# Kernel tuning notes

Hardware: AMD Instinct MI355X
Metric: run time of the kernel (lower is better)

Reference implementation:

```python
import jax, jax.numpy as jnp
import numpy as np

DIM = 128
WINDOW_TOKENS = 64  # window_size**2 = 8*8


def _conv3x3(x, w):
    # x: [B,C,H,W], w: [O,I,3,3], padding=1 (SAME)
    return jax.lax.conv_general_dilated(
        x, w, window_strides=(1, 1), padding='SAME',
        dimension_numbers=('NCHW', 'OIHW', 'NCHW'))


def _pixel_shuffle2(x):
    # torch.nn.PixelShuffle(2): [B, C*4, H, W] -> [B, C, 2H, 2W]
    B, C4, H, W = x.shape
    C = C4 // 4
    x = x.reshape(B, C, 2, 2, H, W)
    x = x.transpose(0, 1, 4, 2, 5, 3)  # [B, C, H, 2, W, 2]
    return x.reshape(B, C, H * 2, W * 2)


def setup_inputs() -> dict:
    key = jax.random.key(0)
    ks = jax.random.split(key, 12)
    B, C = 4, DIM
    f0 = jax.random.normal(ks[0], (B, C, 64, 64), jnp.float32)
    f1 = jax.random.normal(ks[1], (B, C, 128, 128), jnp.float32)
    f2 = jax.random.normal(ks[2], (B, C, 256, 256), jnp.float32)
    s = 0.02
    # Linear weights stored as [in, out] so forward is x @ W
    Wq = jax.random.normal(ks[3], (C, C), jnp.float32) * s
    Wk = jax.random.normal(ks[4], (C, C), jnp.float32) * s
    Wv = jax.random.normal(ks[5], (C, C), jnp.float32) * s
    Wql = jax.random.normal(ks[6], (C, C), jnp.float32) * s
    Wkl = jax.random.normal(ks[7], (C, C), jnp.float32) * s
    Wvl = jax.random.normal(ks[8], (C, C), jnp.float32) * s
    gate_w = jax.random.normal(ks[9], (2 * C, C), jnp.float32) * s
    conv0 = jax.random.normal(ks[10], (4 * C, C, 3, 3), jnp.float32) * s
    conv1 = jax.random.normal(ks[11], (4 * C, C, 3, 3), jnp.float32) * s
    return dict(f0=f0, f1=f1, f2=f2, Wq=Wq, Wk=Wk, Wv=Wv,
                Wql=Wql, Wkl=Wkl, Wvl=Wvl, gate_w=gate_w,
                conv0=conv0, conv1=conv1)


def reference(f0, f1, f2, Wq, Wk, Wv, Wql, Wkl, Wvl, gate_w, conv0, conv1):
    feats = (f0, f1, f2)
    B, C = f0.shape[0], f0.shape[1]
    scale = C ** (-0.5)
    # flatten+concat: [B, N, C]
    toks = [f.reshape(B, C, -1).transpose(0, 2, 1) for f in feats]
    x = jnp.concatenate(toks, axis=1)
    N = x.shape[1]
    wt = WINDOW_TOKENS
    nw = N // wt  # N is divisible by wt for these shapes (no padding)
    windows = x.reshape(B, nw, wt, C)

    # ---- global path (mode='center'): attention over window means ----
    centers = windows.mean(axis=2)  # [B, nw, C]
    Q = centers @ Wq
    K = centers @ Wk
    V = centers @ Wv
    attn = jax.nn.softmax(jnp.einsum('bnc,bmc->bnm', Q, K) * scale, axis=-1)
    y_centers = jnp.einsum('bnm,bmc->bnc', attn, V) * centers
    y_global = jnp.broadcast_to(y_centers[:, :, None, :], (B, nw, wt, C)).reshape(B, N, C)

    # ---- local path: attention within each window (batched over windows) ----
    Ql = windows @ Wql
    Kl = windows @ Wkl
    Vl = windows @ Wvl
    attn_l = jax.nn.softmax(jnp.einsum('bwqc,bwkc->bwqk', Ql, Kl) * scale, axis=-1)
    y_local = (jnp.einsum('bwqk,bwkc->bwqc', attn_l, Vl) * windows).reshape(B, N, C)

    # ---- gated fusion ----
    alpha = jax.nn.sigmoid(jnp.concatenate([y_global, y_local], axis=-1) @ gate_w)
    y = alpha * y_global + (1.0 - alpha) * y_local

    # ---- reshape back to feature maps ----
    maps = []
    start = 0
    for f in feats:
        H, W = f.shape[2], f.shape[3]
        cnt = H * W
        maps.append(y[:, start:start + cnt, :].transpose(0, 2, 1).reshape(B, C, H, W))
        start += cnt
    # ---- inverse wavelet reconstruction (conv3x3 -> pixel shuffle -> add) ----
    outputs = [maps[0]]
    z = maps[0]
    z = _pixel_shuffle2(_conv3x3(z, conv0)) + maps[1]
    outputs.append(z)
    z = _pixel_shuffle2(_conv3x3(z, conv1)) + maps[2]
    outputs.append(z)
    return tuple(outputs)
```

## Files before the change

### kernel.cpp

```cpp
#include <hip/hip_runtime.h>
#include <math.h>

#define WT 64
#define NWIN 1344
#define NP 1408
constexpr float SCALE = 0.088388347648318447f;

#define OUT0 0
#define OUT1 2097152
#define OUT2 10485760

typedef __attribute__((ext_vector_type(8))) short bfrag;
typedef __attribute__((ext_vector_type(8))) _Float16 hfrag;
typedef __attribute__((ext_vector_type(4))) float f32x4;

#define MFMA16 __builtin_amdgcn_mfma_f32_16x16x32_bf16
#define MFMA16H __builtin_amdgcn_mfma_f32_16x16x32_f16

__device__ __forceinline__ unsigned short f2b(float f) {
    union { float f; unsigned u; } v; v.f = f;
    unsigned r = v.u + 0x7fffu + ((v.u >> 16) & 1u);
    return (unsigned short)(r >> 16);
}
__device__ __forceinline__ float b2f(unsigned short u) {
    union { unsigned u; float f; } v; v.u = ((unsigned)u) << 16; return v.f;
}
__device__ __forceinline__ int pack2(float a, float b) {
    return (int)f2b(a) | ((int)f2b(b) << 16);
}

__device__ __forceinline__ bfrag ld256(const char* region, int row, int k) {
    int off = (2 * k) ^ ((row & 7) << 4);
    return *(const bfrag*)(region + row * 256 + off);
}
__device__ __forceinline__ bfrag ld128(const char* region, int row, int k) {
    int off = (2 * k) ^ ((row & 7) << 4);
    return *(const bfrag*)(region + row * 128 + off);
}

__global__ void k_prep(const float* __restrict__ Wql, const float* __restrict__ Wkl,
                       const float* __restrict__ Wvl, const float* __restrict__ gw,
                       const float* __restrict__ Wq, const float* __restrict__ Wk,
                       const float* __restrict__ Wv,
                       unsigned short* __restrict__ MtB,
                       unsigned short* __restrict__ WvltB,
                       unsigned short* __restrict__ G1tB,
                       unsigned short* __restrict__ G0tB,
                       unsigned short* __restrict__ MgtB,
                       unsigned short* __restrict__ WvtB) {
    int n = blockIdx.x, k = threadIdx.x;
    if (blockIdx.y == 0) {
        float a = 0.f;
        for (int c = 0; c < 128; ++c) a += Wkl[n * 128 + c] * Wql[k * 128 + c];
        MtB[n * 128 + k] = f2b(a);
    } else if (blockIdx.y == 1) {
        WvltB[n * 128 + k] = f2b(Wvl[k * 128 + n]);
    } else if (blockIdx.y == 2) {
        G1tB[n * 128 + k] = f2b(gw[(128 + k) * 128 + n]);
    } else if (blockIdx.y == 3) {
        G0tB[n * 128 + k] = f2b(gw[k * 128 + n]);
    } else if (blockIdx.y == 4) {
        float a = 0.f;
        for (int c = 0; c < 128; ++c) a += Wk[n * 128 + c] * Wq[k * 128 + c];
        MgtB[n * 128 + k] = f2b(a);
    } else {
        WvtB[n * 128 + k] = f2b(Wv[k * 128 + n]);
    }
}

__global__ __launch_bounds__(256) void k_prep_conv(
    const float* __restrict__ w0, const float* __restrict__ w1,
    _Float16* __restrict__ W0, _Float16* __restrict__ W1) {
    int idx = blockIdx.x * 256 + threadIdx.x;
    const float* w = blockIdx.y ? w1 : w0;
    _Float16* o = blockIdx.y ? W1 : W0;
    int slice = idx >> 14, rem = idx & 16383;
    int oc = rem >> 5, k = rem & 31;
    int ics = slice / 9, tap = slice - ics * 9;
    o[idx] = (_Float16)w[((size_t)oc * 128 + ics * 32 + k) * 9 + tap];
}

__device__ __forceinline__ void window_src(int n0, const float* f0, const float* f1,
                                           const float* f2, const float*& f, int& p0,
                                           int& HW, int& obase) {
    if (n0 < 4096)        { f = f0; p0 = n0;          HW = 4096;  obase = OUT0; }
    else if (n0 < 20480)  { f = f1; p0 = n0 - 4096;   HW = 16384; obase = OUT1; }
    else                  { f = f2; p0 = n0 - 20480;  HW = 65536; obase = OUT2; }
}

__global__ __launch_bounds__(256) void k_centers(
    const float* __restrict__ f0, const float* __restrict__ f1,
    const float* __restrict__ f2, float* __restrict__ ctr,
    unsigned short* __restrict__ ctrb) {
    int w = blockIdx.x, b = blockIdx.y;
    const float* f; int p0, HW, ob;
    window_src(w * WT, f0, f1, f2, f, p0, HW, ob);
    int lane = threadIdx.x & 63, cg = threadIdx.x >> 6;
    for (int c = cg; c < 128; c += 4) {
        float v = f[(b * 128 + c) * HW + p0 + lane];
        #pragma unroll
        for (int off = 32; off; off >>= 1) v += __shfl_xor(v, off);
        if (lane == 0) {
            float mv = v * (1.0f / 64.0f);
            ctr[(b * NWIN + w) * 128 + c] = mv;
            ctrb[(b * NWIN + w) * 128 + c] = f2b(mv);
        }
    }
}

__global__ __launch_bounds__(256) void k_tgvg2(
    const unsigned short* __restrict__ ctrb, const unsigned short* __restrict__ MgtB,
    const unsigned short* __restrict__ WvtB, unsigned short* __restrict__ Tgb,
    unsigned short* __restrict__ Vgt) {
    int blk = blockIdx.x, b = blockIdx.y;
    int mb = blk * 32;
    int tid = threadIdx.x, wid = tid >> 6, lane = tid & 63;
    int lr = lane & 15, lg = lane >> 4;
    int nb = wid * 32;
    f32x4 tg[2][2] = {};
    f32x4 vg[2][2] = {};
    const unsigned short* Cb = ctrb + ((size_t)b * NWIN + mb) * 128;
    #pragma unroll
    for (int ks = 0; ks < 4; ++ks) {
        int k = ks * 32 + lg * 8;
        bfrag b0 = *(const bfrag*)(Cb + lr * 128 + k);
        bfrag b1 = *(const bfrag*)(Cb + (16 + lr) * 128 + k);
        bfrag m0 = *(const bfrag*)(MgtB + (nb + lr) * 128 + k);
        bfrag m1 = *(const bfrag*)(MgtB + (nb + 16 + lr) * 128 + k);
        bfrag v0 = *(const bfrag*)(WvtB + (nb + lr) * 128 + k);
        bfrag v1 = *(const bfrag*)(WvtB + (nb + 16 + lr) * 128 + k);
        tg[0][0] = MFMA16(m0, b0, tg[0][0], 0, 0, 0);
        tg[0][1] = MFMA16(m0, b1, tg[0][1], 0, 0, 0);
        tg[1][0] = MFMA16(m1, b0, tg[1][0], 0, 0, 0);
        tg[1][1] = MFMA16(m1, b1, tg[1][1], 0, 0, 0);
        vg[0][0] = MFMA16(v0, b0, vg[0][0], 0, 0, 0);
        vg[0][1] = MFMA16(v0, b1, vg[0][1], 0, 0, 0);
        vg[1][0] = MFMA16(v1, b0, vg[1][0], 0, 0, 0);
        vg[1][1] = MFMA16(v1, b1, vg[1][1], 0, 0, 0);
    }
    #pragma unroll
    for (int ni = 0; ni < 2; ++ni)
        #pragma unroll
        for (int mj = 0; mj < 2; ++mj) {
            int n0 = nb + ni * 16 + 4 * lg;
            int m = mb + mj * 16 + lr;
            int2 tv;
            tv.x = pack2(tg[ni][mj][0], tg[ni][mj][1]);
            tv.y = pack2(tg[ni][mj][2], tg[ni][mj][3]);
            *(int2*)(Tgb + ((size_t)b * NWIN + m) * 128 + n0) = tv;
            #pragma unroll
            for (int r = 0; r < 4; ++r)
                Vgt[((size_t)b * 128 + n0 + r) * NP + m] = f2b(vg[ni][mj][r]);
        }
}

__global__ __launch_bounds__(256, 1) void k_qk(
    const unsigned short* __restrict__ Tgb, const unsigned short* __restrict__ ctrb,
    unsigned short* __restrict__ P) {
    extern __shared__ unsigned short Srow[];
    __shared__ float mxs[32], invs[32];
    int blk = blockIdx.x, b = blockIdx.y;
    int mb = blk * 32;
    int tid = threadIdx.x, wid = tid >> 6, lane = tid & 63;
    int lr = lane & 15, lg = lane >> 4;
    int wm = (wid & 1) * 16, wn = (wid >> 1) * 32;

    const unsigned short* Arow = Tgb + ((size_t)b * NWIN + mb + wm + lr) * 128;
    for (int tile = 0; tile < 21; ++tile) {
        int nb = tile * 64 + wn;
        f32x4 acc[2] = {};
        #pragma unroll
        for (int ks = 0; ks < 4; ++ks) {
            int k = ks * 32 + lg * 8;
            bfrag a = *(const bfrag*)(Arow + k);
            #pragma unroll
            for (int nt = 0; nt < 2; ++nt) {
                bfrag bb = *(const bfrag*)(ctrb + ((size_t)b * NWIN + nb + nt * 16 + lr) * 128 + k);
                acc[nt] = MFMA16(a, bb, acc[nt], 0, 0, 0);
            }
        }
        #pragma unroll
        for (int nt = 0; nt < 2; ++nt) {
            int col = nb + nt * 16 + lr;
            #pragma unroll
            for (int r = 0; r < 4; ++r) {
                int mrow = wm + 4 * lg + r;
                Srow[mrow * 1344 + col] = f2b(acc[nt][r]);
            }
        }
    }
    __syncthreads();
    {
        int row = tid >> 3, sub = tid & 7;
        const unsigned short* sr = Srow + row * 1344;
        float mx = -1e30f;
        for (int c = sub; c < 1344; c += 8) mx = fmaxf(mx, b2f(sr[c]));
        mx = fmaxf(mx, __shfl_xor(mx, 1));
        mx = fmaxf(mx, __shfl_xor(mx, 2));
        mx = fmaxf(mx, __shfl_xor(mx, 4));
        float sum = 0.f;
        for (int c = sub; c < 1344; c += 8) sum += __expf((b2f(sr[c]) - mx) * SCALE);
        sum += __shfl_xor(sum, 1);
        sum += __shfl_xor(sum, 2);
        sum += __shfl_xor(sum, 4);
        if (sub == 0) { mxs[row] = mx; invs[row] = 1.0f / sum; }
    }
    __syncthreads();
    unsigned short* Pb = P + ((size_t)b * NWIN + mb) * NP;
    for (int idx = tid; idx < 32 * (NP / 8); idx += 256) {
        int row = idx / (NP / 8), c8 = idx % (NP / 8);
        float mx = mxs[row], inv = invs[row];
        unsigned short o[8];
        #pragma unroll
        for (int e = 0; e < 8; ++e) {
            int c = c8 * 8 + e;
            float p = (c < 1344) ? __expf((b2f(Srow[row * 1344 + c]) - mx) * SCALE) * inv : 0.f;
            o[e] = f2b(p);
        }
        *(int4*)(Pb + row * NP + c8 * 8) = *(int4*)o;
    }
}

__global__ __launch_bounds__(256) void k_pvg0(
    const unsigned short* __restrict__ P, const unsigned short* __restrict__ Vgt,
    const float* __restrict__ ctr, const unsigned short* __restrict__ G0tB,
    float* __restrict__ ycen, float* __restrict__ g0g) {
    __shared__ __align__(16) char Ys[32 * 256];
    int blk = blockIdx.x, b = blockIdx.y;
    int mb = blk * 32;
    int tid = threadIdx.x, wid = tid >> 6, lane = tid & 63;
    int lr = lane & 15, lg = lane >> 4;
    int cb = wid * 32;
    f32x4 acc[2][2] = {};
    const unsigned short* Pb = P + ((size_t)b * NWIN + mb) * NP;
    const unsigned short* Vb = Vgt + (size_t)b * 128 * NP;
    for (int it = 0; it < 44; ++it) {
        int k = it * 32 + lg * 8;
        bfrag a0 = *(const bfrag*)(Vb + (size_t)(cb + lr) * NP + k);
        bfrag a1 = *(const bfrag*)(Vb + (size_t)(cb + 16 + lr) * NP + k);
        bfrag b0 = *(const bfrag*)(Pb + (size_t)lr * NP + k);
        bfrag b1 = *(const bfrag*)(Pb + (size_t)(16 + lr) * NP + k);
        acc[0][0] = MFMA16(a0, b0, acc[0][0], 0, 0, 0);
        acc[0][1] = MFMA16(a0, b1, acc[0][1], 0, 0, 0);
        acc[1][0] = MFMA16(a1, b0, acc[1][0], 0, 0, 0);
        acc[1][1] = MFMA16(a1, b1, acc[1][1], 0, 0, 0);
    }
    #pragma unroll
    for (int ci = 0; ci < 2; ++ci)
        #pragma unroll
        for (int mj = 0; mj < 2; ++mj) {
            int c0 = cb + ci * 16 + 4 * lg;
            int mr = mj * 16 + lr;
            int m = mb + mr;
            size_t base = ((size_t)b * NWIN + m) * 128 + c0;
            float4 cv = *(const float4*)(ctr + base);
            float4 y;
            y.x = acc[ci][mj][0] * cv.x;
            y.y = acc[ci][mj][1] * cv.y;
            y.z = acc[ci][mj][2] * cv.z;
            y.w = acc[ci][mj][3] * cv.w;
            *(float4*)(ycen + base) = y;
            int2 pv; pv.x = pack2(y.x, y.y); pv.y = pack2(y.z, y.w);
            *(int2*)(Ys + mr * 256 + ((2 * c0) ^ ((mr & 7) << 4))) = pv;
        }
    __syncthreads();
    {
        int nb = wid * 32;
        f32x4 g[2][2] = {};
        #pragma unroll
        for (int ks = 0; ks < 4; ++ks) {
            int k = ks * 32 + lg * 8;
            bfrag a0 = *(const bfrag*)(G0tB + (nb + lr) * 128 + k);
            bfrag a1 = *(const bfrag*)(G0tB + (nb + 16 + lr) * 128 + k);
            bfrag b0 = ld256(Ys, lr, k);
            bfrag b1 = ld256(Ys, 16 + lr, k);
            g[0][0] = MFMA16(a0, b0, g[0][0], 0, 0, 0);
            g[0][1] = MFMA16(a0, b1, g[0][1], 0, 0, 0);
            g[1][0] = MFMA16(a1, b0, g[1][0], 0, 0, 0);
            g[1][1] = MFMA16(a1, b1, g[1][1], 0, 0, 0);
        }
        #pragma unroll
        for (int ni = 0; ni < 2; ++ni)
            #pragma unroll
            for (int mj = 0; mj < 2; ++mj) {
                int m = mb + mj * 16 + lr;
                int n0 = nb + ni * 16 + 4 * lg;
                #pragma unroll
                for (int r = 0; r < 4; ++r)
                    g0g[((size_t)b * NWIN + m) * 128 + n0 + r] = g[ni][mj][r];
            }
    }
}

#define XB_OFF 0
#define WT_OFF 16384
#define XM_OFF 49152
#define VT_OFF 65536
#define SMEM_SZ 81920

__global__ __launch_bounds__(256, 2) void k_local_mfma(
    const float* __restrict__ f0, const float* __restrict__ f1,
    const float* __restrict__ f2,
    const unsigned short* __restrict__ MtB,
    const unsigned short* __restrict__ WvltB,
    const unsigned short* __restrict__ G1tB,
    const float* __restrict__ g0g, const float* __restrict__ ycen,
    float* __restrict__ out) {
    extern __shared__ char smem[];
    char* Xb = smem + XB_OFF;
    char* Wt = smem + WT_OFF;
    char* XMb = smem + XM_OFF;
    char* Vt = smem + VT_OFF;

    int w = blockIdx.x, b = blockIdx.y;
    const float* f; int p0, HW, obase;
    window_src(w * WT, f0, f1, f2, f, p0, HW, obase);

    int tid = threadIdx.x;
    int wid = tid >> 6, lane = tid & 63;
    int lr = lane & 15, lg = lane >> 4;

    {
        int t0 = tid & 63, cq = tid >> 6;
        const float* src = f + (size_t)(b * 128 + cq * 32) * HW + p0 + t0;
        float xv[32];
        #pragma unroll
        for (int i = 0; i < 32; ++i) xv[i] = src[(size_t)i * HW];
        int4 wreg[8];
        const int4* wsrc = (const int4*)MtB;
        #pragma unroll
        for (int j = 0; j < 8; ++j) wreg[j] = wsrc[j * 256 + tid];
        #pragma unroll
        for (int j = 0; j < 4; ++j) {
            int c0 = cq * 32 + j * 8;
            int4 v;
            v.x = pack2(xv[j * 8 + 0], xv[j * 8 + 1]);
            v.y = pack2(xv[j * 8 + 2], xv[j * 8 + 3]);
            v.z = pack2(xv[j * 8 + 4], xv[j * 8 + 5]);
            v.w = pack2(xv[j * 8 + 6], xv[j * 8 + 7]);
            *(int4*)(Xb + t0 * 256 + ((2 * c0) ^ ((t0 & 7) << 4))) = v;
        }
        #pragma unroll
        for (int j = 0; j < 8; ++j) {
            int ci = j * 256 + tid, n = ci >> 4, pos = ci & 15;
            *(int4*)(Wt + n * 256 + ((pos * 16) ^ ((n & 7) << 4))) = wreg[j];
        }
    }
    __syncthreads();

    int t = 16 * wid + lr;

    {
        f32x4 acc[8] = {};
        #pragma unroll
        for (int ks = 0; ks < 4; ++ks) {
            int k = ks * 32 + lg * 8;
            bfrag xb = ld256(Xb, t, k);
            #pragma unroll
            for (int ct = 0; ct < 8; ++ct) {
                bfrag am = ld256(Wt, 16 * ct + lr, k);
                acc[ct] = MFMA16(am, xb, acc[ct], 0, 0, 0);
            }
        }
        #pragma unroll
        for (int ct = 0; ct < 8; ++ct) {
            int c0 = 16 * ct + 4 * lg;
            int2 v; v.x = pack2(acc[ct][0], acc[ct][1]); v.y = pack2(acc[ct][2], acc[ct][3]);
            *(int2*)(XMb + t * 256 + ((2 * c0) ^ ((t & 7) << 4))) = v;
        }
    }
    __syncthreads();

    {
        int4 wreg[8];
        const int4* wsrc = (const int4*)WvltB;
        #pragma unroll
        for (int j = 0; j < 8; ++j) wreg[j] = wsrc[j * 256 + tid];

        f32x4 s[4] = {};
        #pragma unroll
        for (int ks = 0; ks < 4; ++ks) {
            int k = ks * 32 + lg * 8;
            bfrag bxm = ld256(XMb, t, k);
            #pragma unroll
            for (int ut = 0; ut < 4; ++ut) {
                bfrag ax = ld256(Xb, 16 * ut + lr, k);
                s[ut] = MFMA16(ax, bxm, s[ut], 0, 0, 0);
            }
        }
        float m = -1e30f;
        #pragma unroll
        for (int ut = 0; ut < 4; ++ut)
            #pragma unroll
            for (int r = 0; r < 4; ++r) m = fmaxf(m, s[ut][r]);
        m = fmaxf(m, __shfl_xor(m, 16));
        m = fmaxf(m, __shfl_xor(m, 32));
        float sum = 0.f;
        float e[4][4];
        #pragma unroll
        for (int ut = 0; ut < 4; ++ut)
            #pragma unroll
            for (int r = 0; r < 4; ++r) {
                e[ut][r] = __expf((s[ut][r] - m) * SCALE);
                sum += e[ut][r];
            }
        sum += __shfl_xor(sum, 16);
        sum += __shfl_xor(sum, 32);
        float pinv = 1.0f / sum;
        #pragma unroll
        for (int ut = 0; ut < 4; ++ut) {
            int u0 = 16 * ut + 4 * lg;
            int2 v;
            v.x = pack2(e[ut][0] * pinv, e[ut][1] * pinv);
            v.y = pack2(e[ut][2] * pinv, e[ut][3] * pinv);
            *(int2*)(XMb + t * 256 + ((2 * u0) ^ ((t & 7) << 4))) = v;
        }
        #pragma unroll
        for (int j = 0; j < 8; ++j) {
            int ci = j * 256 + tid, n = ci >> 4, pos = ci & 15;
            *(int4*)(Wt + n * 256 + ((pos * 16) ^ ((n & 7) << 4))) = wreg[j];
        }
    }
    __syncthreads();

    int4 wregG[8];
    {
        const int4* wsrc = (const int4*)G1tB;
        #pragma unroll
        for (int j = 0; j < 8; ++j) wregG[j] = wsrc[j * 256 + tid];

        f32x4 vacc[8] = {};
        #pragma unroll
        for (int ks = 0; ks < 4; ++ks) {
            int k = ks * 32 + lg * 8;
            bfrag ax = ld256(Xb, t, k);
            #pragma unroll
            for (int ct = 0; ct < 8; ++ct) {
                bfrag bw = ld256(Wt, 16 * ct + lr, k);
                vacc[ct] = MFMA16(ax, bw, vacc[ct], 0, 0, 0);
            }
        }
        #pragma unroll
        for (int ct = 0; ct < 8; ++ct) {
            int c = 16 * ct + lr;
            int u0 = 16 * wid + 4 * lg;
            int2 v; v.x = pack2(vacc[ct][0], vacc[ct][1]); v.y = pack2(vacc[ct][2], vacc[ct][3]);
            *(int2*)(Vt + c * 128 + ((2 * u0) ^ ((c & 7) << 4))) = v;
        }
    }
    __syncthreads();

    float yl[8][4];
    float4 yg4[8], g04[8];
    {
        #pragma unroll
        for (int j = 0; j < 8; ++j) {
            int ci = j * 256 + tid, n = ci >> 4, pos = ci & 15;
            *(int4*)(Wt + n * 256 + ((pos * 16) ^ ((n & 7) << 4))) = wregG[j];
        }
        size_t rbase = ((size_t)b * NWIN + w) * 128 + 4 * lg;
        #pragma unroll
        for (int nt = 0; nt < 8; ++nt) {
            yg4[nt] = *(const float4*)(ycen + rbase + 16 * nt);
            g04[nt] = *(const float4*)(g0g + rbase + 16 * nt);
        }
        f32x4 y[8] = {};
        #pragma unroll
        for (int us = 0; us < 2; ++us) {
            int u = us * 32 + lg * 8;
            bfrag bp = ld256(XMb, t, u);
            #pragma unroll
            for (int ct = 0; ct < 8; ++ct) {
                bfrag av = ld128(Vt, 16 * ct + lr, u);
                y[ct] = MFMA16(av, bp, y[ct], 0, 0, 0);
            }
        }
        #pragma unroll
        for (int ct = 0; ct < 8; ++ct) {
            int c0 = 16 * ct + 4 * lg;
            int2 xw = *(const int2*)(Xb + t * 256 + ((2 * c0) ^ ((t & 7) << 4)));
            float x0 = b2f((unsigned short)(xw.x & 0xffff));
            float x1 = b2f((unsigned short)((unsigned)xw.x >> 16));
            float x2 = b2f((unsigned short)(xw.y & 0xffff));
            float x3 = b2f((unsigned short)((unsigned)xw.y >> 16));
            yl[ct][0] = y[ct][0] * x0;
            yl[ct][1] = y[ct][1] * x1;
            yl[ct][2] = y[ct][2] * x2;
            yl[ct][3] = y[ct][3] * x3;
            int2 v; v.x = pack2(yl[ct][0], yl[ct][1]); v.y = pack2(yl[ct][2], yl[ct][3]);
            *(int2*)(Xb + t * 256 + ((2 * c0) ^ ((t & 7) << 4))) = v;
        }
    }
    __syncthreads();

    {
        f32x4 g[8] = {};
        #pragma unroll
        for (int ks = 0; ks < 4; ++ks) {
            int k = ks * 32 + lg * 8;
            bfrag byl = ld256(Xb, t, k);
            #pragma unroll
            for (int nt = 0; nt < 8; ++nt) {
                bfrag ag = ld256(Wt, 16 * nt + lr, k);
                g[nt] = MFMA16(ag, byl, g[nt], 0, 0, 0);
            }
        }
        #pragma unroll
        for (int nt = 0; nt < 8; ++nt) {
            float gv[4] = {g04[nt].x, g04[nt].y, g04[nt].z, g04[nt].w};
            float yv4[4] = {yg4[nt].x, yg4[nt].y, yg4[nt].z, yg4[nt].w};
            #pragma unroll
            for (int r = 0; r < 4; ++r) {
                int c = 16 * nt + 4 * lg + r;
                float a = 1.0f / (1.0f + __expf(-(g[nt][r] + gv[r])));
                float yv = a * yv4[r] + (1.0f - a) * yl[nt][r];
                out[obase + (size_t)(b * 128 + c) * HW + p0 + t] = yv;
            }
        }
    }
}

template <int H, int W>
__global__ __launch_bounds__(256, 2) void k_conv_mfma(
    const float* __restrict__ in, const _Float16* __restrict__ Wcv,
    float* __restrict__ out) {
    constexpr int TXN = W / 32;
    int tile = blockIdx.x;
    int ty = tile / TXN, tx = tile % TXN;
    int y0 = ty * 4, x0 = tx * 32;
    int ob = blockIdx.y * 256;
    int b = blockIdx.z;

    __shared__ __align__(16) char sXs[16384];

    int tid = threadIdx.x;
    int wid = tid >> 6, lane = tid & 63;
    int lr = lane & 15, lg = lane >> 4;

    f32x4 acc[8][4] = {};

    int sy = tid / 34, sx = tid - sy * 34;
    int gy = y0 + sy - 1, gx = x0 + sx - 1;
    bool act = tid < 204;
    bool ok = act && gy >= 0 && gy < H && gx >= 0 && gx < W;
    const float* gp = in + (size_t)b * 128 * H * W + (size_t)gy * W + gx;
    int xswz = (tid >> 3) & 1;

    const _Float16* wbase = Wcv + (size_t)(ob + lr) * 32 + lg * 8;

    hfrag afC[4], afN[4];
    #pragma unroll
    for (int n = 0; n < 4; ++n)
        afC[n] = *(const hfrag*)(wbase + (size_t)(wid * 4 + n) * 512);

    if (act) {
        float xv[32];
        if (ok) {
            #pragma unroll
            for (int ic = 0; ic < 32; ++ic) xv[ic] = gp[(size_t)ic * H * W];
        } else {
            #pragma unroll
            for (int ic = 0; ic < 32; ++ic) xv[ic] = 0.f;
        }
        #pragma unroll
        for (int s = 0; s < 4; ++s) {
            _Float16 hh[8];
            #pragma unroll
            for (int e = 0; e < 8; ++e) hh[e] = (_Float16)xv[s * 8 + e];
            *(int4*)(sXs + tid * 80 + ((s ^ xswz) << 4)) = *(int4*)hh;
        }
    }
    __syncthreads();

    for (int ics = 0; ics < 4; ++ics) {
        if (ics) {
            __syncthreads();
            if (act) {
                float xv[32];
                if (ok) {
                    #pragma unroll
                    for (int ic = 0; ic < 32; ++ic)
                        xv[ic] = gp[(size_t)(ics * 32 + ic) * H * W];
                } else {
                    #pragma unroll
                    for (int ic = 0; ic < 32; ++ic) xv[ic] = 0.f;
                }
                #pragma unroll
                for (int s = 0; s < 4; ++s) {
                    _Float16 hh[8];
                    #pragma unroll
                    for (int e = 0; e < 8; ++e) hh[e] = (_Float16)xv[s * 8 + e];
                    *(int4*)(sXs + tid * 80 + ((s ^ xswz) << 4)) = *(int4*)hh;
                }
            }
            __syncthreads();
        }
        #pragma unroll
        for (int tap = 0; tap < 9; ++tap) {
            int kg = ics * 9 + tap;
            if (tap < 8 || ics < 3) {
                const _Float16* ws = wbase + (size_t)(kg + 1) * 16384;
                #pragma unroll
                for (int n = 0; n < 4; ++n)
                    afN[n] = *(const hfrag*)(ws + (size_t)(wid * 4 + n) * 512);
            }
            int dy = tap / 3, dx = tap - dy * 3;
            hfrag bf[8];
            #pragma unroll
            for (int m = 0; m < 8; ++m) {
                int row = ((m >> 1) + dy) * 34 + (m & 1) * 16 + lr + dx;
                bf[m] = *(const hfrag*)(sXs + row * 80 + ((lg ^ ((row >> 3) & 1)) << 4));
            }
            #pragma unroll
            for (int m = 0; m < 8; ++m)
                #pragma unroll
                for (int n = 0; n < 4; ++n)
                    acc[m][n] = MFMA16H(afC[n], bf[m], acc[m][n], 0, 0, 0);
            #pragma unroll
            for (int n = 0; n < 4; ++n) afC[n] = afN[n];
        }
    }

    float* outb = out + (size_t)b * 128 * 4 * H * W;
    #pragma unroll
    for (int n = 0; n < 4; ++n) {
        int oc0 = ob + (wid * 4 + n) * 16 + lg * 4;
        int c = oc0 >> 2;
        #pragma unroll
        for (int mr = 0; mr < 4; ++mr) {
            int py = y0 + mr;
            #pragma unroll
            for (int i2 = 0; i2 < 2; ++i2) {
                size_t rowb = ((size_t)c * (2 * H) + 2 * py + i2) * (2 * W);
                float2* p0 = (float2*)(outb + rowb + 2 * (x0 + lr));
                float2 v0 = *p0;
                v0.x += acc[2 * mr][n][i2 * 2 + 0];
                v0.y += acc[2 * mr][n][i2 * 2 + 1];
                *p0 = v0;
                float2* p1 = (float2*)(outb + rowb + 2 * (x0 + 16 + lr));
                float2 v1 = *p1;
                v1.x += acc[2 * mr + 1][n][i2 * 2 + 0];
                v1.y += acc[2 * mr + 1][n][i2 * 2 + 1];
                *p1 = v1;
            }
        }
    }
}

extern "C" void kernel_launch(void* const* d_in, const int* in_sizes, int n_in,
                              void* d_out, int out_size, void* d_ws, size_t ws_size,
                              hipStream_t stream) {
    const float* f0 = (const float*)d_in[0];
    const float* f1 = (const float*)d_in[1];
    const float* f2 = (const float*)d_in[2];
    const float* Wq = (const float*)d_in[3];
    const float* Wk = (const float*)d_in[4];
    const float* Wv = (const float*)d_in[5];
    const float* Wql = (const float*)d_in[6];
    const float* Wkl = (const float*)d_in[7];
    const float* Wvl = (const float*)d_in[8];
    const float* gate_w = (const float*)d_in[9];
    const float* conv0 = (const float*)d_in[10];
    const float* conv1 = (const float*)d_in[11];
    float* out = (float*)d_out;
    float* ws = (float*)d_ws;

    float* ctr = ws;
    float* ycen = ctr + 688128;
    float* g0g = ycen + 688128;
    unsigned short* MtB = (unsigned short*)(g0g + 688128);
    unsigned short* WvltB = MtB + 16384;
    unsigned short* G1tB = WvltB + 16384;
    unsigned short* G0tB = G1tB + 16384;
    unsigned short* MgtB = G0tB + 16384;
    unsigned short* WvtB = MgtB + 16384;
    _Float16* Wcv0 = (_Float16*)(WvtB + 16384);
    _Float16* Wcv1 = Wcv0 + 589824;
    unsigned short* ctrb = (unsigned short*)(Wcv1 + 589824);
    unsigned short* Tgb = ctrb + 688128;
    unsigned short* Vgt = Tgb + 688128;
    unsigned short* Pg = Vgt + 4 * 128 * NP;

    hipFuncSetAttribute((const void*)k_local_mfma,
                        hipFuncAttributeMaxDynamicSharedMemorySize, SMEM_SZ);
    hipFuncSetAttribute((const void*)k_qk,
                        hipFuncAttributeMaxDynamicSharedMemorySize, 32 * 1344 * 2);

    k_prep<<<dim3(128, 6), 128, 0, stream>>>(Wql, Wkl, Wvl, gate_w, Wq, Wk, Wv,
                                             MtB, WvltB, G1tB, G0tB, MgtB, WvtB);
    k_prep_conv<<<dim3(2304, 2), 256, 0, stream>>>(conv0, conv1, Wcv0, Wcv1);
    k_centers<<<dim3(NWIN, 4), 256, 0, stream>>>(f0, f1, f2, ctr, ctrb);
    k_tgvg2<<<dim3(NWIN / 32, 4), 256, 0, stream>>>(ctrb, MgtB, WvtB, Tgb, Vgt);
    k_qk<<<dim3(NWIN / 32, 4), 256, 32 * 1344 * 2, stream>>>(Tgb, ctrb, Pg);
    k_pvg0<<<dim3(NWIN / 32, 4), 256, 0, stream>>>(Pg, Vgt, ctr, G0tB, ycen, g0g);
    k_local_mfma<<<dim3(NWIN, 4), 256, SMEM_SZ, stream>>>(
        f0, f1, f2, MtB, WvltB, G1tB, g0g, ycen, out);
    k_conv_mfma<64, 64><<<dim3(32, 2, 4), 256, 0, stream>>>(out + OUT0, Wcv0, out + OUT1);
    k_conv_mfma<128, 128><<<dim3(128, 2, 4), 256, 0, stream>>>(out + OUT1, Wcv1, out + OUT2);
}
```

Measured before the change: 568.7 us.

## Fuse global-path QK, softmax and PV into one kernel keeping P in LDS

Merges the global attention score, softmax and PV+gate kernels into a single kernel that keeps the probability matrix in shared memory. The Q·M projection is now computed in-block into LDS instead of being written to a global Tgb buffer. This removes the global round trips for P and Tgb and one kernel launch. In exchange it uses more LDS per block, pads the row stride to reduce bank conflicts, and serializes the stages within a block. This global path is a small part of total time, which is dominated by the local and conv kernels.

```diff
diff --git a/kernel.cpp b/kernel.cpp
--- a/kernel.cpp
+++ b/kernel.cpp
@@ -4,6 +4,7 @@
 #define WT 64
 #define NWIN 1344
 #define NP 1408
+#define SROW_STRIDE 1352
 constexpr float SCALE = 0.088388347648318447f;
 
 #define OUT0 0
@@ -108,16 +109,14 @@
     }
 }
 
-__global__ __launch_bounds__(256) void k_tgvg2(
-    const unsigned short* __restrict__ ctrb, const unsigned short* __restrict__ MgtB,
-    const unsigned short* __restrict__ WvtB, unsigned short* __restrict__ Tgb,
+__global__ __launch_bounds__(256) void k_vg(
+    const unsigned short* __restrict__ ctrb, const unsigned short* __restrict__ WvtB,
     unsigned short* __restrict__ Vgt) {
     int blk = blockIdx.x, b = blockIdx.y;
     int mb = blk * 32;
     int tid = threadIdx.x, wid = tid >> 6, lane = tid & 63;
     int lr = lane & 15, lg = lane >> 4;
     int nb = wid * 32;
-    f32x4 tg[2][2] = {};
     f32x4 vg[2][2] = {};
     const unsigned short* Cb = ctrb + ((size_t)b * NWIN + mb) * 128;
     #pragma unroll
@@ -125,14 +124,8 @@
         int k = ks * 32 + lg * 8;
         bfrag b0 = *(const bfrag*)(Cb + lr * 128 + k);
         bfrag b1 = *(const bfrag*)(Cb + (16 + lr) * 128 + k);
-        bfrag m0 = *(const bfrag*)(MgtB + (nb + lr) * 128 + k);
-        bfrag m1 = *(const bfrag*)(MgtB + (nb + 16 + lr) * 128 + k);
         bfrag v0 = *(const bfrag*)(WvtB + (nb + lr) * 128 + k);
         bfrag v1 = *(const bfrag*)(WvtB + (nb + 16 + lr) * 128 + k);
-        tg[0][0] = MFMA16(m0, b0, tg[0][0], 0, 0, 0);
-        tg[0][1] = MFMA16(m0, b1, tg[0][1], 0, 0, 0);
-        tg[1][0] = MFMA16(m1, b0, tg[1][0], 0, 0, 0);
-        tg[1][1] = MFMA16(m1, b1, tg[1][1], 0, 0, 0);
         vg[0][0] = MFMA16(v0, b0, vg[0][0], 0, 0, 0);
         vg[0][1] = MFMA16(v0, b1, vg[0][1], 0, 0, 0);
         vg[1][0] = MFMA16(v1, b0, vg[1][0], 0, 0, 0);
@@ -144,55 +137,86 @@
         for (int mj = 0; mj < 2; ++mj) {
             int n0 = nb + ni * 16 + 4 * lg;
             int m = mb + mj * 16 + lr;
-            int2 tv;
-            tv.x = pack2(tg[ni][mj][0], tg[ni][mj][1]);
-            tv.y = pack2(tg[ni][mj][2], tg[ni][mj][3]);
-            *(int2*)(Tgb + ((size_t)b * NWIN + m) * 128 + n0) = tv;
             #pragma unroll
             for (int r = 0; r < 4; ++r)
                 Vgt[((size_t)b * 128 + n0 + r) * NP + m] = f2b(vg[ni][mj][r]);
         }
 }
 
-__global__ __launch_bounds__(256, 1) void k_qk(
-    const unsigned short* __restrict__ Tgb, const unsigned short* __restrict__ ctrb,
-    unsigned short* __restrict__ P) {
-    extern __shared__ unsigned short Srow[];
+#define QKPV_LDS (32 * SROW_STRIDE * 2 + 8192)
+
+__global__ __launch_bounds__(256, 1) void k_qkpv(
+    const unsigned short* __restrict__ ctrb, const unsigned short* __restrict__ MgtB,
+    const unsigned short* __restrict__ Vgt, const unsigned short* __restrict__ G0tB,
+    const float* __restrict__ ctr, float* __restrict__ ycen,
+    float* __restrict__ g0g) {
+    extern __shared__ char smem2[];
+    unsigned short* Srow = (unsigned short*)smem2;
+    char* Ys = smem2 + 32 * SROW_STRIDE * 2;
     __shared__ float mxs[32], invs[32];
     int blk = blockIdx.x, b = blockIdx.y;
     int mb = blk * 32;
     int tid = threadIdx.x, wid = tid >> 6, lane = tid & 63;
     int lr = lane & 15, lg = lane >> 4;
-    int wm = (wid & 1) * 16, wn = (wid >> 1) * 32;
-
-    const unsigned short* Arow = Tgb + ((size_t)b * NWIN + mb + wm + lr) * 128;
-    for (int tile = 0; tile < 21; ++tile) {
-        int nb = tile * 64 + wn;
-        f32x4 acc[2] = {};
+
+    {
+        int nb = wid * 32;
+        f32x4 tg[2][2] = {};
+        const unsigned short* Cb = ctrb + ((size_t)b * NWIN + mb) * 128;
         #pragma unroll
         for (int ks = 0; ks < 4; ++ks) {
             int k = ks * 32 + lg * 8;
-            bfrag a = *(const bfrag*)(Arow + k);
+            bfrag b0 = *(const bfrag*)(Cb + lr * 128 + k);
+            bfrag b1 = *(const bfrag*)(Cb + (16 + lr) * 128 + k);
+            bfrag m0 = *(const bfrag*)(MgtB + (nb + lr) * 128 + k);
+            bfrag m1 = *(const bfrag*)(MgtB + (nb + 16 + lr) * 128 + k);
+            tg[0][0] = MFMA16(m0, b0, tg[0][0], 0, 0, 0);
+            tg[0][1] = MFMA16(m0, b1, tg[0][1], 0, 0, 0);
+            tg[1][0] = MFMA16(m1, b0, tg[1][0], 0, 0, 0);
+            tg[1][1] = MFMA16(m1, b1, tg[1][1], 0, 0, 0);
+        }
+        #pragma unroll
+        for (int ni = 0; ni < 2; ++ni)
+            #pragma unroll
+            for (int mj = 0; mj < 2; ++mj) {
+                int n0 = nb + ni * 16 + 4 * lg;
+                int m = mj * 16 + lr;
+                int2 v; v.x = pack2(tg[ni][mj][0], tg[ni][mj][1]);
+                v.y = pack2(tg[ni][mj][2], tg[ni][mj][3]);
+                *(int2*)(Ys + m * 256 + ((2 * n0) ^ ((m & 7) << 4))) = v;
+            }
+    }
+    __syncthreads();
+
+    {
+        int wm = (wid & 1) * 16, wn = (wid >> 1) * 32;
+        for (int tile = 0; tile < 21; ++tile) {
+            int nb = tile * 64 + wn;
+            f32x4 acc[2] = {};
+            #pragma unroll
+            for (int ks = 0; ks < 4; ++ks) {
+                int k = ks * 32 + lg * 8;
+                bfrag a = ld256(Ys, wm + lr, k);
+                #pragma unroll
+                for (int nt = 0; nt < 2; ++nt) {
+                    bfrag bb = *(const bfrag*)(ctrb + ((size_t)b * NWIN + nb + nt * 16 + lr) * 128 + k);
+                    acc[nt] = MFMA16(a, bb, acc[nt], 0, 0, 0);
+                }
+            }
             #pragma unroll
             for (int nt = 0; nt < 2; ++nt) {
-                bfrag bb = *(const bfrag*)(ctrb + ((size_t)b * NWIN + nb + nt * 16 + lr) * 128 + k);
-                acc[nt] = MFMA16(a, bb, acc[nt], 0, 0, 0);
-            }
-        }
-        #pragma unroll
-        for (int nt = 0; nt < 2; ++nt) {
-            int col = nb + nt * 16 + lr;
-            #pragma unroll
-            for (int r = 0; r < 4; ++r) {
-                int mrow = wm + 4 * lg + r;
-                Srow[mrow * 1344 + col] = f2b(acc[nt][r]);
-            }
-        }
-    }
-    __syncthreads();
+                int col = nb + nt * 16 + lr;
+                #pragma unroll
+                for (int r = 0; r < 4; ++r)
+                    Srow[(wm + 4 * lg + r) * SROW_STRIDE + col] = f2b(acc[nt][r]);
+            }
+        }
+    }
+    __syncthreads();
+
     {
         int row = tid >> 3, sub = tid & 7;
-        const unsigned short* sr = Srow + row * 1344;
+        const unsigned short* sr = Srow + row * SROW_STRIDE;
         float mx = -1e30f;
         for (int c = sub; c < 1344; c += 8) mx = fmaxf(mx, b2f(sr[c]));
         mx = fmaxf(mx, __shfl_xor(mx, 1));
@@ -206,64 +230,57 @@
         if (sub == 0) { mxs[row] = mx; invs[row] = 1.0f / sum; }
     }
     __syncthreads();
-    unsigned short* Pb = P + ((size_t)b * NWIN + mb) * NP;
-    for (int idx = tid; idx < 32 * (NP / 8); idx += 256) {
-        int row = idx / (NP / 8), c8 = idx % (NP / 8);
+    for (int idx = tid; idx < 32 * (SROW_STRIDE / 8); idx += 256) {
+        int row = idx / (SROW_STRIDE / 8), c8 = idx % (SROW_STRIDE / 8);
         float mx = mxs[row], inv = invs[row];
+        unsigned short* sp = Srow + row * SROW_STRIDE + c8 * 8;
         unsigned short o[8];
         #pragma unroll
         for (int e = 0; e < 8; ++e) {
             int c = c8 * 8 + e;
-            float p = (c < 1344) ? __expf((b2f(Srow[row * 1344 + c]) - mx) * SCALE) * inv : 0.f;
+            float p = (c < 1344) ? __expf((b2f(sp[e]) - mx) * SCALE) * inv : 0.f;
             o[e] = f2b(p);
         }
-        *(int4*)(Pb + row * NP + c8 * 8) = *(int4*)o;
-    }
-}
-
-__global__ __launch_bounds__(256) void k_pvg0(
-    const unsigned short* __restrict__ P, const unsigned short* __restrict__ Vgt,
-    const float* __restrict__ ctr, const unsigned short* __restrict__ G0tB,
-    float* __restrict__ ycen, float* __restrict__ g0g) {
-    __shared__ __align__(16) char Ys[32 * 256];
-    int blk = blockIdx.x, b = blockIdx.y;
-    int mb = blk * 32;
-    int tid = threadIdx.x, wid = tid >> 6, lane = tid & 63;
-    int lr = lane & 15, lg = lane >> 4;
-    int cb = wid * 32;
-    f32x4 acc[2][2] = {};
-    const unsigned short* Pb = P + ((size_t)b * NWIN + mb) * NP;
-    const unsigned short* Vb = Vgt + (size_t)b * 128 * NP;
-    for (int it = 0; it < 44; ++it) {
-        int k = it * 32 + lg * 8;
-        bfrag a0 = *(const bfrag*)(Vb + (size_t)(cb + lr) * NP + k);
-        bfrag a1 = *(const bfrag*)(Vb + (size_t)(cb + 16 + lr) * NP + k);
-        bfrag b0 = *(const bfrag*)(Pb + (size_t)lr * NP + k);
-        bfrag b1 = *(const bfrag*)(Pb + (size_t)(16 + lr) * NP + k);
-        acc[0][0] = MFMA16(a0, b0, acc[0][0], 0, 0, 0);
-        acc[0][1] = MFMA16(a0, b1, acc[0][1], 0, 0, 0);
-        acc[1][0] = MFMA16(a1, b0, acc[1][0], 0, 0, 0);
-        acc[1][1] = MFMA16(a1, b1, acc[1][1], 0, 0, 0);
-    }
-    #pragma unroll
-    for (int ci = 0; ci < 2; ++ci)
-        #pragma unroll
-        for (int mj = 0; mj < 2; ++mj) {
-            int c0 = cb + ci * 16 + 4 * lg;
-            int mr = mj * 16 + lr;
-            int m = mb + mr;
-            size_t base = ((size_t)b * NWIN + m) * 128 + c0;
-            float4 cv = *(const float4*)(ctr + base);
-            float4 y;
-            y.x = acc[ci][mj][0] * cv.x;
-            y.y = acc[ci][mj][1] * cv.y;
-            y.z = acc[ci][mj][2] * cv.z;
-            y.w = acc[ci][mj][3] * cv.w;
-            *(float4*)(ycen + base) = y;
-            int2 pv; pv.x = pack2(y.x, y.y); pv.y = pack2(y.z, y.w);
-            *(int2*)(Ys + mr * 256 + ((2 * c0) ^ ((mr & 7) << 4))) = pv;
-        }
-    __syncthreads();
+        *(int4*)sp = *(int4*)o;
+    }
+    __syncthreads();
+
+    {
+        int cb = wid * 32;
+        f32x4 acc[2][2] = {};
+        const unsigned short* Vb = Vgt + (size_t)b * 128 * NP;
+        for (int it = 0; it < 42; ++it) {
+            int k = it * 32 + lg * 8;
+            bfrag a0 = *(const bfrag*)(Vb + (size_t)(cb + lr) * NP + k);
+            bfrag a1 = *(const bfrag*)(Vb + (size_t)(cb + 16 + lr) * NP + k);
+            bfrag b0 = *(const bfrag*)(Srow + lr * SROW_STRIDE + k);
+            bfrag b1 = *(const bfrag*)(Srow + (16 + lr) * SROW_STRIDE + k);
+            acc[0][0] = MFMA16(a0, b0, acc[0][0], 0, 0, 0);
+            acc[0][1] = MFMA16(a0, b1, acc[0][1], 0, 0, 0);
+            acc[1][0] = MFMA16(a1, b0, acc[1][0], 0, 0, 0);
+            acc[1][1] = MFMA16(a1, b1, acc[1][1], 0, 0, 0);
+        }
+        #pragma unroll
+        for (int ci = 0; ci < 2; ++ci)
+            #pragma unroll
+            for (int mj = 0; mj < 2; ++mj) {
+                int c0 = cb + ci * 16 + 4 * lg;
+                int mr = mj * 16 + lr;
+                int m = mb + mr;
+                size_t base = ((size_t)b * NWIN + m) * 128 + c0;
+                float4 cv = *(const float4*)(ctr + base);
+                float4 y;
+                y.x = acc[ci][mj][0] * cv.x;
+                y.y = acc[ci][mj][1] * cv.y;
+                y.z = acc[ci][mj][2] * cv.z;
+                y.w = acc[ci][mj][3] * cv.w;
+                *(float4*)(ycen + base) = y;
+                int2 pv; pv.x = pack2(y.x, y.y); pv.y = pack2(y.z, y.w);
+                *(int2*)(Ys + mr * 256 + ((2 * c0) ^ ((mr & 7) << 4))) = pv;
+            }
+    }
+    __syncthreads();
+
     {
         int nb = wid * 32;
         f32x4 g[2][2] = {};
@@ -677,22 +694,20 @@
     _Float16* Wcv0 = (_Float16*)(WvtB + 16384);
     _Float16* Wcv1 = Wcv0 + 589824;
     unsigned short* ctrb = (unsigned short*)(Wcv1 + 589824);
-    unsigned short* Tgb = ctrb + 688128;
-    unsigned short* Vgt = Tgb + 688128;
-    unsigned short* Pg = Vgt + 4 * 128 * NP;
+    unsigned short* Vgt = ctrb + 688128;
 
     hipFuncSetAttribute((const void*)k_local_mfma,
                         hipFuncAttributeMaxDynamicSharedMemorySize, SMEM_SZ);
-    hipFuncSetAttribute((const void*)k_qk,
-                        hipFuncAttributeMaxDynamicSharedMemorySize, 32 * 1344 * 2);
+    hipFuncSetAttribute((const void*)k_qkpv,
+                        hipFuncAttributeMaxDynamicSharedMemorySize, QKPV_LDS);
 
     k_prep<<<dim3(128, 6), 128, 0, stream>>>(Wql, Wkl, Wvl, gate_w, Wq, Wk, Wv,
                                              MtB, WvltB, G1tB, G0tB, MgtB, WvtB);
     k_prep_conv<<<dim3(2304, 2), 256, 0, stream>>>(conv0, conv1, Wcv0, Wcv1);
     k_centers<<<dim3(NWIN, 4), 256, 0, stream>>>(f0, f1, f2, ctr, ctrb);
-    k_tgvg2<<<dim3(NWIN / 32, 4), 256, 0, stream>>>(ctrb, MgtB, WvtB, Tgb, Vgt);
-    k_qk<<<dim3(NWIN / 32, 4), 256, 32 * 1344 * 2, stream>>>(Tgb, ctrb, Pg);
-    k_pvg0<<<dim3(NWIN / 32, 4), 256, 0, stream>>>(Pg, Vgt, ctr, G0tB, ycen, g0g);
+    k_vg<<<dim3(NWIN / 32, 4), 256, 0, stream>>>(ctrb, WvtB, Vgt);
+    k_qkpv<<<dim3(NWIN / 32, 4), 256, QKPV_LDS, stream>>>(
+        ctrb, MgtB, Vgt, G0tB, ctr, ycen, g0g);
     k_local_mfma<<<dim3(NWIN, 4), 256, SMEM_SZ, stream>>>(
         f0, f1, f2, MtB, WvltB, G1tB, g0g, ycen, out);
     k_conv_mfma<64, 64><<<dim3(32, 2, 4), 256, 0, stream>>>(out + OUT0, Wcv0, out + OUT1);
```

New measurement: 549.4 us. 1.04x faster.
